# Kernel optimization log

Hardware: AMD Instinct MI355X
Metric: run time of the kernel (lower is better)

The kernel has to match this reference:

```python
import jax, jax.numpy as jnp
import numpy as np

K = 8  # avg_kernel (pool kernel == stride, and nearest-upsample factor)


def conv1x1(u, W, b):
    # 1x1 conv == per-pixel linear map over channels
    return jnp.einsum('bchw,oc->bohw', u, W) + b[None, :, None, None]


def setup_inputs() -> dict:
    key = jax.random.key(0)
    ks = jax.random.split(key, 9)
    C = 64
    x = jax.random.normal(ks[0], (8, C, 512, 512), dtype=jnp.float32)
    def w(k):
        return jax.random.normal(k, (C, C), dtype=jnp.float32) * 0.05
    def bias(k):
        return jax.random.normal(k, (C,), dtype=jnp.float32) * 0.05
    return {
        'x': x,
        'Wt': w(ks[1]), 'bt': bias(ks[2]),
        'Wp': w(ks[3]), 'bp': bias(ks[4]),
        'Wg': w(ks[5]), 'bg': bias(ks[6]),
        'Wc': w(ks[7]), 'bc': bias(ks[8]),
    }


def reference(x, Wt, bt, Wp, bp, Wg, bg, Wc, bc):
    B, C, H, W = x.shape
    # AvgPool2d(kernel=K, stride=K): exact reshape-mean since H,W divisible by K
    u = x.reshape(B, C, H // K, K, W // K, K).mean(axis=(3, 5))  # [B,C,h,w]
    b_, c_, h, w_ = u.shape
    N = h * w_
    theta = conv1x1(u, Wt, bt).reshape(B, C, N).transpose(0, 2, 1)  # [B,N,C]
    phi = conv1x1(u, Wp, bp).reshape(B, C, N)                       # [B,C,N] (downsample = flatten)
    g = conv1x1(u, Wg, bg).reshape(B, C, N).transpose(0, 2, 1)      # [B,N,C]
    attn = jax.nn.softmax(jnp.einsum('bnc,bcm->bnm', theta, phi), axis=-1)  # [B,N,N], unscaled
    y = jnp.einsum('bnm,bmc->bnc', attn, g)                         # [B,N,C]
    y = y.transpose(0, 2, 1).reshape(B, C, h, w_)
    y = conv1x1(y, Wc, bc)
    # F.interpolate(size=[H,W]) default nearest; integer factor K -> exact repeat
    y = jnp.repeat(jnp.repeat(y, K, axis=2), K, axis=3)
    return y
```

## Files before the change

kernel.cpp:

```cpp
#include <hip/hip_runtime.h>
#include <hip/hip_bf16.h>


typedef short short8 __attribute__((ext_vector_type(8)));
typedef float floatx4 __attribute__((ext_vector_type(4)));

__device__ inline unsigned short f2bf(float f) {
    union { float f; unsigned int u; } v; v.f = f;
    unsigned int u = v.u;
    u += 0x7fff + ((u >> 16) & 1);
    return (unsigned short)(u >> 16);
}

__global__ __launch_bounds__(256) void k_pool(const float* __restrict__ x,
                                              float* __restrict__ u) {
    int id = blockIdx.x * 256 + threadIdx.x;
    int ow = id & 63;
    int oh = (id >> 6) & 63;
    int bc = id >> 12;
    const float* p = x + ((size_t)bc * 512 + oh * 8) * 512 + ow * 8;
    float s = 0.f;
#pragma unroll
    for (int r = 0; r < 8; ++r) {
        const float4* q = (const float4*)(p + r * 512);
        float4 a = q[0], b = q[1];
        s += a.x + a.y + a.z + a.w + b.x + b.y + b.z + b.w;
    }
    u[id] = s * (1.f / 64.f);
}

__global__ __launch_bounds__(256) void k_qkv(const float* __restrict__ u,
    const float* __restrict__ Wt, const float* __restrict__ bt,
    const float* __restrict__ Wp, const float* __restrict__ bp,
    const float* __restrict__ Wg, const float* __restrict__ bg,
    unsigned short* __restrict__ th, unsigned short* __restrict__ ph,
    unsigned short* __restrict__ gT) {
    __shared__ float U[64 * 66];
    __shared__ float WtT[64 * 64];
    __shared__ float WpT[64 * 64];
    int b = blockIdx.x >> 6;
    int n0 = (blockIdx.x & 63) * 64;
    int t = threadIdx.x;
#pragma unroll
    for (int i = 0; i < 4; ++i) {
        int f4 = t + 256 * i;
        int cin = f4 >> 4, pos = f4 & 15;
        float4 v = *(const float4*)(u + ((size_t)(b * 64 + cin)) * 4096 + n0 + pos * 4);
        U[cin * 66 + pos * 4 + 0] = v.x;
        U[cin * 66 + pos * 4 + 1] = v.y;
        U[cin * 66 + pos * 4 + 2] = v.z;
        U[cin * 66 + pos * 4 + 3] = v.w;
    }
#pragma unroll
    for (int i = 0; i < 16; ++i) {
        int idx = t + 256 * i;
        int co = idx & 63, ci = idx >> 6;
        WtT[ci * 64 + co] = Wt[co * 64 + ci];
        WpT[ci * 64 + co] = Wp[co * 64 + ci];
    }
    __syncthreads();
    int cO = t & 63, wv = t >> 6;
#pragma unroll 4
    for (int i = 0; i < 16; ++i) {
        int nl = wv + 4 * i;
        float at = bt[cO], ap = bp[cO];
#pragma unroll
        for (int cin = 0; cin < 64; ++cin) {
            float uv = U[cin * 66 + nl];
            at += WtT[cin * 64 + cO] * uv;
            ap += WpT[cin * 64 + cO] * uv;
        }
        size_t o = ((size_t)(b * 4096 + n0 + nl)) * 64 + cO;
        th[o] = f2bf(at);
        ph[o] = f2bf(ap);
    }
#pragma unroll 4
    for (int i = 0; i < 16; ++i) {
        int c = wv + 4 * i;
        float ag = bg[c];
#pragma unroll
        for (int cin = 0; cin < 64; ++cin)
            ag += Wg[c * 64 + cin] * U[cin * 66 + (t & 63)];
        gT[((size_t)(b * 64 + c)) * 4096 + n0 + (t & 63)] = f2bf(ag);
    }
}

__global__ __launch_bounds__(256) void k_attn(
    const unsigned short* __restrict__ th,
    const unsigned short* __restrict__ ph,
    const unsigned short* __restrict__ gT,
    float* __restrict__ y) {
    __shared__ unsigned short Th[64 * 72];
    __shared__ unsigned short Ph[64 * 72];
    __shared__ unsigned short Gt[64 * 72];
    __shared__ unsigned short Pl[4 * 16 * 72];
    int b = blockIdx.x >> 6;
    int n0 = (blockIdx.x & 63) * 64;
    int t = threadIdx.x;
    int wave = t >> 6, lane = t & 63, quad = lane >> 4, l16 = lane & 15;
    int row = t >> 2, cg = t & 3;

    {
        const unsigned short* src = th + ((size_t)(b * 4096 + n0 + row)) * 64;
        *(short8*)(Th + row * 72 + cg * 8)      = *(const short8*)(src + cg * 8);
        *(short8*)(Th + row * 72 + 32 + cg * 8) = *(const short8*)(src + 32 + cg * 8);
    }
    __syncthreads();
    short8 a0 = *(const short8*)(Th + (wave * 16 + l16) * 72 + quad * 8);
    short8 a1 = *(const short8*)(Th + (wave * 16 + l16) * 72 + 32 + quad * 8);

    floatx4 Yacc[4];
#pragma unroll
    for (int ct = 0; ct < 4; ++ct) Yacc[ct] = (floatx4){0.f, 0.f, 0.f, 0.f};
    float l[4] = {0.f, 0.f, 0.f, 0.f};

    for (int mt = 0; mt < 64; ++mt) {
        __syncthreads();
        int m0 = mt * 64;
        {
            const unsigned short* sp = ph + ((size_t)(b * 4096 + m0 + row)) * 64;
            *(short8*)(Ph + row * 72 + cg * 8)      = *(const short8*)(sp + cg * 8);
            *(short8*)(Ph + row * 72 + 32 + cg * 8) = *(const short8*)(sp + 32 + cg * 8);
            const unsigned short* sg = gT + ((size_t)(b * 64 + row)) * 4096 + m0;
            *(short8*)(Gt + row * 72 + cg * 8)      = *(const short8*)(sg + cg * 8);
            *(short8*)(Gt + row * 72 + 32 + cg * 8) = *(const short8*)(sg + 32 + cg * 8);
        }
        __syncthreads();

        floatx4 P[4];
        float psum[4] = {0.f, 0.f, 0.f, 0.f};
#pragma unroll
        for (int ct = 0; ct < 4; ++ct) {
            short8 b0 = *(const short8*)(Ph + (ct * 16 + l16) * 72 + quad * 8);
            short8 b1 = *(const short8*)(Ph + (ct * 16 + l16) * 72 + 32 + quad * 8);
            floatx4 acc = (floatx4){0.f, 0.f, 0.f, 0.f};
            acc = __builtin_amdgcn_mfma_f32_16x16x32_bf16(a0, b0, acc, 0, 0, 0);
            acc = __builtin_amdgcn_mfma_f32_16x16x32_bf16(a1, b1, acc, 0, 0, 0);
#pragma unroll
            for (int r = 0; r < 4; ++r) {
                float e = __expf(acc[r]);
                P[ct][r] = e;
                psum[r] += e;
            }
        }
#pragma unroll
        for (int off = 1; off < 16; off <<= 1)
#pragma unroll
            for (int r = 0; r < 4; ++r) psum[r] += __shfl_xor(psum[r], off);
#pragma unroll
        for (int r = 0; r < 4; ++r) l[r] += psum[r];
#pragma unroll
        for (int ct = 0; ct < 4; ++ct)
#pragma unroll
            for (int r = 0; r < 4; ++r)
                Pl[wave * 16 * 72 + (quad * 4 + r) * 72 + ct * 16 + l16] = f2bf(P[ct][r]);
        short8 p0 = *(const short8*)(Pl + wave * 16 * 72 + l16 * 72 + quad * 8);
        short8 p1 = *(const short8*)(Pl + wave * 16 * 72 + l16 * 72 + 32 + quad * 8);
#pragma unroll
        for (int ct = 0; ct < 4; ++ct) {
            short8 g0 = *(const short8*)(Gt + (ct * 16 + l16) * 72 + quad * 8);
            short8 g1 = *(const short8*)(Gt + (ct * 16 + l16) * 72 + 32 + quad * 8);
            Yacc[ct] = __builtin_amdgcn_mfma_f32_16x16x32_bf16(p0, g0, Yacc[ct], 0, 0, 0);
            Yacc[ct] = __builtin_amdgcn_mfma_f32_16x16x32_bf16(p1, g1, Yacc[ct], 0, 0, 0);
        }
    }
#pragma unroll
    for (int ct = 0; ct < 4; ++ct)
#pragma unroll
        for (int r = 0; r < 4; ++r) {
            int rr = n0 + wave * 16 + quad * 4 + r;
            y[((size_t)(b * 4096 + rr)) * 64 + ct * 16 + l16] = Yacc[ct][r] / l[r];
        }
}

__global__ __launch_bounds__(256) void k_out(const float* __restrict__ y,
    const float* __restrict__ Wc, const float* __restrict__ bc,
    float* __restrict__ out) {
    __shared__ float Y[64 * 66];
    int b = blockIdx.x >> 6;
    int oh = blockIdx.x & 63;
    int t = threadIdx.x;
#pragma unroll
    for (int i = 0; i < 4; ++i) {
        int f4 = t + 256 * i;
        int w = f4 >> 4, cgp = f4 & 15;
        float4 v = *(const float4*)(y + ((size_t)(b * 4096 + oh * 64 + w)) * 64 + cgp * 4);
        Y[(cgp * 4 + 0) * 66 + w] = v.x;
        Y[(cgp * 4 + 1) * 66 + w] = v.y;
        Y[(cgp * 4 + 2) * 66 + w] = v.z;
        Y[(cgp * 4 + 3) * 66 + w] = v.w;
    }
    __syncthreads();
    int w = t & 63, wv = t >> 6;
#pragma unroll 2
    for (int i = 0; i < 16; ++i) {
        int c = wv + 4 * i;
        float acc = bc[c];
#pragma unroll
        for (int cin = 0; cin < 64; ++cin)
            acc += Wc[c * 64 + cin] * Y[cin * 66 + w];
        float4 v4 = {acc, acc, acc, acc};
        float* base = out + (((size_t)(b * 64 + c)) * 512 + oh * 8) * 512 + w * 8;
#pragma unroll
        for (int r = 0; r < 8; ++r) {
            *(float4*)(base + (size_t)r * 512) = v4;
            *(float4*)(base + (size_t)r * 512 + 4) = v4;
        }
    }
}

extern "C" void kernel_launch(void* const* d_in, const int* in_sizes, int n_in,
                              void* d_out, int out_size, void* d_ws, size_t ws_size,
                              hipStream_t stream) {
    const float* x  = (const float*)d_in[0];
    const float* Wt = (const float*)d_in[1];
    const float* bt = (const float*)d_in[2];
    const float* Wp = (const float*)d_in[3];
    const float* bp = (const float*)d_in[4];
    const float* Wg = (const float*)d_in[5];
    const float* bg = (const float*)d_in[6];
    const float* Wc = (const float*)d_in[7];
    const float* bc = (const float*)d_in[8];
    float* out = (float*)d_out;
    char* ws = (char*)d_ws;
    float* u            = (float*)(ws);
    unsigned short* th  = (unsigned short*)(ws + (8  << 20));
    unsigned short* ph  = (unsigned short*)(ws + (12 << 20));
    unsigned short* gT  = (unsigned short*)(ws + (16 << 20));
    float* y            = (float*)(ws + (20 << 20));

    hipLaunchKernelGGL(k_pool, dim3(8192), dim3(256), 0, stream, x, u);
    hipLaunchKernelGGL(k_qkv,  dim3(512),  dim3(256), 0, stream,
                       u, Wt, bt, Wp, bp, Wg, bg, th, ph, gT);
    hipLaunchKernelGGL(k_attn, dim3(512),  dim3(256), 0, stream, th, ph, gT, y);
    hipLaunchKernelGGL(k_out,  dim3(512),  dim3(256), 0, stream, y, Wc, bc, out);
}
```

Baseline: 1.285 ms.

## Double-buffer attention K/V tiles with register prefetch and DPP row sums

The attention kernel now double-buffers the phi and g tiles in shared memory. The next tile is loaded from global memory into registers at the top of each iteration and written to the alternate buffer after the MFMAs, which leaves one barrier per iteration instead of two. The softmax row-sum reduction switches from shfl_xor to DPP row_shr adds. It also raises wave priority with s_setprio around the MFMA blocks and writes the P tile to LDS inline. The cost is twice the LDS for the phi and g tiles and more live registers, which could lower occupancy; the last iteration also prefetches a wrapped-around tile that is never used.

Result: faster. 1.244 ms (-3.2%).

```diff
diff --git a/kernel.cpp b/kernel.cpp
--- a/kernel.cpp
+++ b/kernel.cpp
@@ -10,6 +10,14 @@
     unsigned int u = v.u;
     u += 0x7fff + ((u >> 16) & 1);
     return (unsigned short)(u >> 16);
+}
+
+__device__ inline float rowsum16(float x) {
+    x += __int_as_float(__builtin_amdgcn_update_dpp(0, __float_as_int(x), 0x121, 0xf, 0xf, false));
+    x += __int_as_float(__builtin_amdgcn_update_dpp(0, __float_as_int(x), 0x122, 0xf, 0xf, false));
+    x += __int_as_float(__builtin_amdgcn_update_dpp(0, __float_as_int(x), 0x124, 0xf, 0xf, false));
+    x += __int_as_float(__builtin_amdgcn_update_dpp(0, __float_as_int(x), 0x128, 0xf, 0xf, false));
+    return x;
 }
 
 __global__ __launch_bounds__(256) void k_pool(const float* __restrict__ x,
@@ -91,8 +99,8 @@
     const unsigned short* __restrict__ gT,
     float* __restrict__ y) {
     __shared__ unsigned short Th[64 * 72];
-    __shared__ unsigned short Ph[64 * 72];
-    __shared__ unsigned short Gt[64 * 72];
+    __shared__ unsigned short Ph[2][64 * 72];
+    __shared__ unsigned short Gt[2][64 * 72];
     __shared__ unsigned short Pl[4 * 16 * 72];
     int b = blockIdx.x >> 6;
     int n0 = (blockIdx.x & 63) * 64;
@@ -104,6 +112,12 @@
         const unsigned short* src = th + ((size_t)(b * 4096 + n0 + row)) * 64;
         *(short8*)(Th + row * 72 + cg * 8)      = *(const short8*)(src + cg * 8);
         *(short8*)(Th + row * 72 + 32 + cg * 8) = *(const short8*)(src + 32 + cg * 8);
+        const unsigned short* sp = ph + ((size_t)(b * 4096 + row)) * 64;
+        *(short8*)(Ph[0] + row * 72 + cg * 8)      = *(const short8*)(sp + cg * 8);
+        *(short8*)(Ph[0] + row * 72 + 32 + cg * 8) = *(const short8*)(sp + 32 + cg * 8);
+        const unsigned short* sg = gT + ((size_t)(b * 64 + row)) * 4096;
+        *(short8*)(Gt[0] + row * 72 + cg * 8)      = *(const short8*)(sg + cg * 8);
+        *(short8*)(Gt[0] + row * 72 + 32 + cg * 8) = *(const short8*)(sg + 32 + cg * 8);
     }
     __syncthreads();
     short8 a0 = *(const short8*)(Th + (wave * 16 + l16) * 72 + quad * 8);
@@ -114,55 +128,59 @@
     for (int ct = 0; ct < 4; ++ct) Yacc[ct] = (floatx4){0.f, 0.f, 0.f, 0.f};
     float l[4] = {0.f, 0.f, 0.f, 0.f};
 
+    int cur = 0;
     for (int mt = 0; mt < 64; ++mt) {
-        __syncthreads();
-        int m0 = mt * 64;
+        int mn = ((mt + 1) & 63) * 64;
+        short8 r0, r1, r2, r3;
         {
-            const unsigned short* sp = ph + ((size_t)(b * 4096 + m0 + row)) * 64;
-            *(short8*)(Ph + row * 72 + cg * 8)      = *(const short8*)(sp + cg * 8);
-            *(short8*)(Ph + row * 72 + 32 + cg * 8) = *(const short8*)(sp + 32 + cg * 8);
-            const unsigned short* sg = gT + ((size_t)(b * 64 + row)) * 4096 + m0;
-            *(short8*)(Gt + row * 72 + cg * 8)      = *(const short8*)(sg + cg * 8);
-            *(short8*)(Gt + row * 72 + 32 + cg * 8) = *(const short8*)(sg + 32 + cg * 8);
-        }
-        __syncthreads();
-
-        floatx4 P[4];
+            const unsigned short* sp = ph + ((size_t)(b * 4096 + mn + row)) * 64;
+            r0 = *(const short8*)(sp + cg * 8);
+            r1 = *(const short8*)(sp + 32 + cg * 8);
+            const unsigned short* sg = gT + ((size_t)(b * 64 + row)) * 4096 + mn;
+            r2 = *(const short8*)(sg + cg * 8);
+            r3 = *(const short8*)(sg + 32 + cg * 8);
+        }
+        const unsigned short* PhC = Ph[cur];
+        const unsigned short* GtC = Gt[cur];
+
         float psum[4] = {0.f, 0.f, 0.f, 0.f};
 #pragma unroll
         for (int ct = 0; ct < 4; ++ct) {
-            short8 b0 = *(const short8*)(Ph + (ct * 16 + l16) * 72 + quad * 8);
-            short8 b1 = *(const short8*)(Ph + (ct * 16 + l16) * 72 + 32 + quad * 8);
+            short8 b0 = *(const short8*)(PhC + (ct * 16 + l16) * 72 + quad * 8);
+            short8 b1 = *(const short8*)(PhC + (ct * 16 + l16) * 72 + 32 + quad * 8);
             floatx4 acc = (floatx4){0.f, 0.f, 0.f, 0.f};
+            __builtin_amdgcn_s_setprio(1);
             acc = __builtin_amdgcn_mfma_f32_16x16x32_bf16(a0, b0, acc, 0, 0, 0);
             acc = __builtin_amdgcn_mfma_f32_16x16x32_bf16(a1, b1, acc, 0, 0, 0);
+            __builtin_amdgcn_s_setprio(0);
 #pragma unroll
             for (int r = 0; r < 4; ++r) {
                 float e = __expf(acc[r]);
-                P[ct][r] = e;
                 psum[r] += e;
+                Pl[wave * 16 * 72 + (quad * 4 + r) * 72 + ct * 16 + l16] = f2bf(e);
             }
         }
 #pragma unroll
-        for (int off = 1; off < 16; off <<= 1)
-#pragma unroll
-            for (int r = 0; r < 4; ++r) psum[r] += __shfl_xor(psum[r], off);
-#pragma unroll
-        for (int r = 0; r < 4; ++r) l[r] += psum[r];
-#pragma unroll
-        for (int ct = 0; ct < 4; ++ct)
-#pragma unroll
-            for (int r = 0; r < 4; ++r)
-                Pl[wave * 16 * 72 + (quad * 4 + r) * 72 + ct * 16 + l16] = f2bf(P[ct][r]);
+        for (int r = 0; r < 4; ++r) l[r] += rowsum16(psum[r]);
         short8 p0 = *(const short8*)(Pl + wave * 16 * 72 + l16 * 72 + quad * 8);
         short8 p1 = *(const short8*)(Pl + wave * 16 * 72 + l16 * 72 + 32 + quad * 8);
+        __builtin_amdgcn_s_setprio(1);
 #pragma unroll
         for (int ct = 0; ct < 4; ++ct) {
-            short8 g0 = *(const short8*)(Gt + (ct * 16 + l16) * 72 + quad * 8);
-            short8 g1 = *(const short8*)(Gt + (ct * 16 + l16) * 72 + 32 + quad * 8);
+            short8 g0 = *(const short8*)(GtC + (ct * 16 + l16) * 72 + quad * 8);
+            short8 g1 = *(const short8*)(GtC + (ct * 16 + l16) * 72 + 32 + quad * 8);
             Yacc[ct] = __builtin_amdgcn_mfma_f32_16x16x32_bf16(p0, g0, Yacc[ct], 0, 0, 0);
             Yacc[ct] = __builtin_amdgcn_mfma_f32_16x16x32_bf16(p1, g1, Yacc[ct], 0, 0, 0);
         }
+        __builtin_amdgcn_s_setprio(0);
+        unsigned short* PhN = Ph[cur ^ 1];
+        unsigned short* GtN = Gt[cur ^ 1];
+        *(short8*)(PhN + row * 72 + cg * 8)      = r0;
+        *(short8*)(PhN + row * 72 + 32 + cg * 8) = r1;
+        *(short8*)(GtN + row * 72 + cg * 8)      = r2;
+        *(short8*)(GtN + row * 72 + 32 + cg * 8) = r3;
+        __syncthreads();
+        cur ^= 1;
     }
 #pragma unroll
     for (int ct = 0; ct < 4; ++ct)
```
